# Performance work log

Measured on AMD Instinct MI355X. Metric: run time of the kernel, lower is better.

## Reference

```python
import jax, jax.numpy as jnp
import numpy as np

TOKENS = 32768
D_MODEL = 4096
N_EXPERTS = 64
BALANCE_LOSS_WEIGHT = 0.1


def setup_inputs() -> dict:
    key = jax.random.key(0)
    kx, kw1, kw2, kn = jax.random.split(key, 4)
    x = jax.random.normal(kx, (TOKENS, D_MODEL), dtype=jnp.float32)
    # torch nn.Linear weight layout: [out_features, in_features]
    w1 = jax.random.normal(kw1, (N_EXPERTS, D_MODEL), dtype=jnp.float32) / np.sqrt(D_MODEL)
    w2 = jax.random.normal(kw2, (N_EXPERTS, N_EXPERTS), dtype=jnp.float32) / np.sqrt(N_EXPERTS)
    # fixed Gumbel noise sample: g = -log(-log(u)), matching gumbel_rsample
    u = jax.random.uniform(kn, (TOKENS, N_EXPERTS), dtype=jnp.float32, minval=1e-8, maxval=1.0)
    noise = -jnp.log(-jnp.log(u))
    return {"x": x, "w1": w1, "w2": w2, "noise": noise}


def reference(x, w1, w2, noise):
    # MLP gate: Linear(d->E, no bias) -> tanh -> Linear(E->E, no bias)
    h = jnp.tanh(x @ w1.T)                       # [T, E]
    logits = h @ w2.T                             # [T, E]
    scores = jax.nn.softmax(logits, axis=1)       # [T, E]
    logits_w_noise = logits + noise               # gumbel-perturbed logits
    top1_indices = jnp.argmax(logits_w_noise, axis=1)   # [T] int
    top1_scores = jnp.max(logits_w_noise, axis=1)       # [T]
    # balance loss
    importance_mean = scores.mean(axis=0)                        # [E]
    load = jnp.bincount(top1_indices, length=N_EXPERTS)          # [E] int
    load_mean = load.astype(scores.dtype) / x.shape[0]           # [E]
    balance_loss = (N_EXPERTS * jnp.sum(importance_mean * load_mean)
                    * BALANCE_LOSS_WEIGHT)
    return (top1_indices, top1_scores, balance_loss, load_mean, importance_mean)
```

## Files before the change

### kernel.cpp

```cpp
#include <hip/hip_runtime.h>
#include <math.h>

#define TOKENS 32768
#define DM 4096
#define NE 64
#define BALW 0.1f

#define TG 64
#define GBLOCKS (TOKENS / TG)

typedef __attribute__((ext_vector_type(8))) short short8;
typedef __attribute__((ext_vector_type(4))) float f32x4;

typedef unsigned short us;

__device__ inline us bf16r(float f) {
  const unsigned u = __float_as_uint(f);
  return (us)((u + 0x7FFFu + ((u >> 16) & 1u)) >> 16);
}
__device__ inline float bf16f(us s) {
  return __uint_as_float(((unsigned)s) << 16);
}
__device__ inline void split8(const float4 v0, const float4 v1, short8& H,
                              short8& M, short8& L) {
  float v[8] = {v0.x, v0.y, v0.z, v0.w, v1.x, v1.y, v1.z, v1.w};
#pragma unroll
  for (int j = 0; j < 8; ++j) {
    const us hs = bf16r(v[j]);
    const float r1 = v[j] - bf16f(hs);
    const us ms = bf16r(r1);
    const float r2 = r1 - bf16f(ms);
    const us ls = bf16r(r2);
    H[j] = (short)hs; M[j] = (short)ms; L[j] = (short)ls;
  }
}

__device__ inline void split8t(const float4 v0, const float4 v1, short8& H,
                               short8& M, short8& L) {
  unsigned u[8], um[8], ul[8];
  const float v[8] = {v0.x, v0.y, v0.z, v0.w, v1.x, v1.y, v1.z, v1.w};
#pragma unroll
  for (int j = 0; j < 8; ++j) {
    u[j] = __float_as_uint(v[j]);
    const float r1 = v[j] - __uint_as_float(u[j] & 0xFFFF0000u);
    um[j] = __float_as_uint(r1);
    const float r2 = r1 - __uint_as_float(um[j] & 0xFFFF0000u);
    ul[j] = __float_as_uint(r2);
  }
  union Cvt { unsigned u4[4]; short8 s8; } h, m, l;
#pragma unroll
  for (int d = 0; d < 4; ++d) {
    h.u4[d] = __builtin_amdgcn_perm(u[2 * d + 1], u[2 * d], 0x07060302u);
    m.u4[d] = __builtin_amdgcn_perm(um[2 * d + 1], um[2 * d], 0x07060302u);
    l.u4[d] = __builtin_amdgcn_perm(ul[2 * d + 1], ul[2 * d], 0x07060302u);
  }
  H = h.s8; M = m.s8; L = l.s8;
}

#define MFMA(a, b, c) __builtin_amdgcn_mfma_f32_16x16x32_bf16(a, b, c, 0, 0, 0)

__global__ void prep_w1_kernel(const float* __restrict__ w1,
                               us* __restrict__ bws) {
  const int kc = blockIdx.x;
  const int tid = threadIdx.x;
  const int ns = tid >> 6;
  const int l = tid & 63;
  const int r = l & 15, g = l >> 4;
  const int n = 16 * ns + r;
  const int kb = 32 * kc + 8 * g;
  const float* src = &w1[(size_t)n * DM + kb];
  const float4 v0 = *reinterpret_cast<const float4*>(src);
  const float4 v1 = *reinterpret_cast<const float4*>(src + 4);
  short8 H, M, L;
  split8(v0, v1, H, M, L);
  us* dst = bws + ((size_t)(kc * 4 + ns) * 3) * 512 + l * 8;
  *reinterpret_cast<short8*>(dst) = H;
  *reinterpret_cast<short8*>(dst + 512) = M;
  *reinterpret_cast<short8*>(dst + 1024) = L;
}

#define TMM 128

template <int SK>
__global__ __launch_bounds__(256, 2) void gemm_mfma_kernel(
    const float* __restrict__ x, const us* __restrict__ bws,
    float* __restrict__ hp) {
  constexpr int KS = DM / SK;
  constexpr int NIT = KS / 32;
  const int tid = threadIdx.x;
  const int kz = blockIdx.x % SK;
  const int mb = blockIdx.x / SK;
  const int w = tid >> 6;
  const int l = tid & 63;
  const int r = l & 15, g = l >> 4;
  const int row0 = mb * TMM + w * 32;
  const int kb0 = kz * KS;

  f32x4 acc[2][4];
#pragma unroll
  for (int i = 0; i < 2; ++i)
#pragma unroll
    for (int j = 0; j < 4; ++j) acc[i][j] = (f32x4)(0.f);

  const float* xA0 = &x[(size_t)(row0 + r) * DM + kb0 + 8 * g];
  const float* xA1 = xA0 + (size_t)16 * DM;
  const us* bb = bws + (size_t)(kb0 / 32) * 12 * 512 + l * 8;

  float4 a00 = *reinterpret_cast<const float4*>(xA0);
  float4 a01 = *reinterpret_cast<const float4*>(xA0 + 4);
  float4 a10 = *reinterpret_cast<const float4*>(xA1);
  float4 a11 = *reinterpret_cast<const float4*>(xA1 + 4);
  short8 bf[4][3];
#pragma unroll
  for (int ns = 0; ns < 4; ++ns)
#pragma unroll
    for (int p = 0; p < 3; ++p)
      bf[ns][p] = *reinterpret_cast<const short8*>(bb + (ns * 3 + p) * 512);

  for (int it = 0; it < NIT; ++it) {
    const int itn = (it + 1 < NIT) ? it + 1 : it;
    const us* btn = bb + (size_t)itn * 12 * 512;
    const int ko = itn * 32;
    const float4 n00 = *reinterpret_cast<const float4*>(xA0 + ko);
    const float4 n01 = *reinterpret_cast<const float4*>(xA0 + ko + 4);
    const float4 n10 = *reinterpret_cast<const float4*>(xA1 + ko);
    const float4 n11 = *reinterpret_cast<const float4*>(xA1 + ko + 4);

    short8 ah0, am0, al0, ah1, am1, al1;
    split8t(a00, a01, ah0, am0, al0);
    split8t(a10, a11, ah1, am1, al1);

#define PROW(AH0, AH1, P)                                                \
  do {                                                                   \
    _Pragma("unroll") for (int ns = 0; ns < 4; ++ns) {                   \
      acc[0][ns] = MFMA(AH0, bf[ns][P], acc[0][ns]);                     \
      acc[1][ns] = MFMA(AH1, bf[ns][P], acc[1][ns]);                     \
    }                                                                    \
  } while (0)
#define RELOAD(P)                                                        \
  do {                                                                   \
    _Pragma("unroll") for (int ns = 0; ns < 4; ++ns) bf[ns][P] =         \
        *reinterpret_cast<const short8*>(btn + (ns * 3 + (P)) * 512);    \
  } while (0)

    PROW(ah0, ah1, 0);
    PROW(am0, am1, 0);
    PROW(al0, al1, 0);
    RELOAD(0);
    PROW(ah0, ah1, 1);
    PROW(am0, am1, 1);
    RELOAD(1);
    PROW(ah0, ah1, 2);
    RELOAD(2);
#undef PROW
#undef RELOAD

    a00 = n00; a01 = n01; a10 = n10; a11 = n11;
  }

  float* dst = hp + (size_t)kz * TOKENS * NE;
#pragma unroll
  for (int ms = 0; ms < 2; ++ms)
#pragma unroll
    for (int ns = 0; ns < 4; ++ns)
#pragma unroll
      for (int q = 0; q < 4; ++q)
        dst[(size_t)(row0 + 16 * ms + 4 * g + q) * NE + 16 * ns + r] =
            acc[ms][ns][q];
}

#define TM 128
#define BK 32
#define LDSA 132
#define LDSB 68

template <int SK>
__global__ __launch_bounds__(256, 4) void gemm_fp32_kernel(
    const float* __restrict__ x, const float* __restrict__ w1,
    float* __restrict__ hp) {
  constexpr int KS = DM / SK;
  __shared__ float As[BK * LDSA];
  __shared__ float Ws[BK * LDSB];
  const int tid = threadIdx.x;
  const int kz = blockIdx.x % SK;
  const int mb = blockIdx.x / SK;
  const int row0 = mb * TM;
  const int kbase = kz * KS;
  const int m0 = (tid >> 3) * 4;
  const int n0 = (tid & 7) * 8;
  const int rS = tid >> 2;
  const int kS = (tid & 3) * 4;

  float acc[4][8];
#pragma unroll
  for (int i = 0; i < 4; ++i)
#pragma unroll
    for (int j = 0; j < 8; ++j) acc[i][j] = 0.f;

  float4 ra[4], rw[2];
  const float* xp = &x[(size_t)(row0 + rS) * DM + kS];
  const float* wp = &w1[(size_t)rS * DM + kS];

#define LOAD_TILE(KC)                                                   \
  do {                                                                  \
    ra[0] = *reinterpret_cast<const float4*>(xp + (KC));                \
    ra[1] = *reinterpret_cast<const float4*>(xp + (KC) + 16);           \
    ra[2] = *reinterpret_cast<const float4*>(xp + (size_t)64 * DM + (KC));\
    ra[3] = *reinterpret_cast<const float4*>(xp + (size_t)64 * DM + (KC) + 16);\
    rw[0] = *reinterpret_cast<const float4*>(wp + (KC));                \
    rw[1] = *reinterpret_cast<const float4*>(wp + (KC) + 16);           \
  } while (0)

#define ST4(arr, stride, krow, col, v)                                  \
  do {                                                                  \
    arr[((krow) + 0) * (stride) + (col)] = (v).x;                       \
    arr[((krow) + 1) * (stride) + (col)] = (v).y;                       \
    arr[((krow) + 2) * (stride) + (col)] = (v).z;                       \
    arr[((krow) + 3) * (stride) + (col)] = (v).w;                       \
  } while (0)

#define STORE_TILE()                                                    \
  do {                                                                  \
    ST4(As, LDSA, kS, rS, ra[0]);                                       \
    ST4(As, LDSA, kS + 16, rS, ra[1]);                                  \
    ST4(As, LDSA, kS, rS + 64, ra[2]);                                  \
    ST4(As, LDSA, kS + 16, rS + 64, ra[3]);                             \
    ST4(Ws, LDSB, kS, rS, rw[0]);                                       \
    ST4(Ws, LDSB, kS + 16, rS, rw[1]);                                  \
  } while (0)

  LOAD_TILE(kbase);

  for (int kc = kbase; kc < kbase + KS; kc += BK) {
    __syncthreads();
    STORE_TILE();
    __syncthreads();
    if (kc + BK < kbase + KS) LOAD_TILE(kc + BK);
#pragma unroll 8
    for (int k = 0; k < BK; ++k) {
      const float4 a0 = *reinterpret_cast<const float4*>(&As[k * LDSA + m0]);
      const float4 b0 = *reinterpret_cast<const float4*>(&Ws[k * LDSB + n0]);
      const float4 b1 =
          *reinterpret_cast<const float4*>(&Ws[k * LDSB + n0 + 4]);
      const float a[4] = {a0.x, a0.y, a0.z, a0.w};
      const float b[8] = {b0.x, b0.y, b0.z, b0.w, b1.x, b1.y, b1.z, b1.w};
#pragma unroll
      for (int i = 0; i < 4; ++i)
#pragma unroll
        for (int j = 0; j < 8; ++j) acc[i][j] = fmaf(a[i], b[j], acc[i][j]);
    }
  }
#undef LOAD_TILE
#undef ST4
#undef STORE_TILE

  float* dst = hp + (size_t)kz * TOKENS * NE;
#pragma unroll
  for (int i = 0; i < 4; ++i) {
    const size_t o = (size_t)(row0 + m0 + i) * NE;
    *reinterpret_cast<float4*>(&dst[o + n0]) =
        make_float4(acc[i][0], acc[i][1], acc[i][2], acc[i][3]);
    *reinterpret_cast<float4*>(&dst[o + n0 + 4]) =
        make_float4(acc[i][4], acc[i][5], acc[i][6], acc[i][7]);
  }
}

template <int SK>
__global__ __launch_bounds__(256) void gate_kernel(
    const float* __restrict__ hp, const float* __restrict__ w2,
    const float* __restrict__ noise, float* __restrict__ out_idx,
    float* __restrict__ out_score, float* __restrict__ imp_part,
    float* __restrict__ load_part) {
  __shared__ float hs[TG * 65];
  __shared__ float w2s[NE * 65];
  __shared__ float ls[TG * 66];
  __shared__ float csum[2 * NE];
  __shared__ int hist[NE];
  const int tid = threadIdx.x;
  const int t0 = blockIdx.x * TG;
  if (tid < NE) hist[tid] = 0;

#pragma unroll
  for (int it = 0; it < 4; ++it) {
    const int f = tid + 256 * it;
    const int c = f & 15;
    const int t = f >> 4;
    const size_t g = (size_t)(t0 + t) * NE + c * 4;
    float4 p = *reinterpret_cast<const float4*>(&hp[g]);
#pragma unroll
    for (int s = 1; s < SK; ++s) {
      const float4 q =
          *reinterpret_cast<const float4*>(&hp[(size_t)s * TOKENS * NE + g]);
      p.x += q.x; p.y += q.y; p.z += q.z; p.w += q.w;
    }
    float* d = &hs[t * 65 + c * 4];
    d[0] = tanhf(p.x);
    d[1] = tanhf(p.y);
    d[2] = tanhf(p.z);
    d[3] = tanhf(p.w);
  }
#pragma unroll
  for (int it = 0; it < 4; ++it) {
    const int f = tid + 256 * it;
    const int c = f & 15;
    const int rr = f >> 4;
    const float4 v =
        *reinterpret_cast<const float4*>(&w2[(size_t)rr * NE + c * 4]);
    float* d = &w2s[rr * 65 + c * 4];
    d[0] = v.x; d[1] = v.y; d[2] = v.z; d[3] = v.w;
  }
  __syncthreads();

  {
    const int m0 = (tid >> 4) * 4;
    const int n0 = (tid & 15) * 4;
    float acc[4][4];
#pragma unroll
    for (int i = 0; i < 4; ++i)
#pragma unroll
      for (int j = 0; j < 4; ++j) acc[i][j] = 0.f;
#pragma unroll 8
    for (int k = 0; k < NE; ++k) {
      float a[4], b[4];
#pragma unroll
      for (int i = 0; i < 4; ++i) a[i] = hs[(m0 + i) * 65 + k];
#pragma unroll
      for (int j = 0; j < 4; ++j) b[j] = w2s[(n0 + j) * 65 + k];
#pragma unroll
      for (int i = 0; i < 4; ++i)
#pragma unroll
        for (int j = 0; j < 4; ++j) acc[i][j] = fmaf(a[i], b[j], acc[i][j]);
    }
#pragma unroll
    for (int i = 0; i < 4; ++i)
#pragma unroll
      for (int j = 0; j < 4; ++j) ls[(m0 + i) * 66 + n0 + j] = acc[i][j];
  }
  __syncthreads();

  if (tid < TG) {
    const int t = tid;
    float mx = -INFINITY, best = -INFINITY;
    int bi = 0;
    for (int e = 0; e < NE; ++e) {
      const float lv = ls[t * 66 + e];
      mx = fmaxf(mx, lv);
      const float gg = lv + noise[(size_t)(t0 + t) * NE + e];
      if (gg > best) { best = gg; bi = e; }
    }
    float s = 0.f;
    for (int e = 0; e < NE; ++e) {
      const float ex = expf(ls[t * 66 + e] - mx);
      s += ex;
      ls[t * 66 + e] = ex;
    }
    const float inv = 1.f / s;
    for (int e = 0; e < NE; ++e) ls[t * 66 + e] *= inv;
    out_idx[t0 + t] = (float)bi;
    out_score[t0 + t] = best;
    atomicAdd(&hist[bi], 1);
  }
  __syncthreads();

  if (tid < 128) {
    const int e = tid & 63;
    const int half = tid >> 6;
    float s = 0.f;
    for (int rr = half * 32; rr < half * 32 + 32; ++rr) s += ls[rr * 66 + e];
    csum[half * NE + e] = s;
  }
  __syncthreads();
  if (tid < NE) {
    imp_part[(size_t)blockIdx.x * NE + tid] = csum[tid] + csum[NE + tid];
    load_part[(size_t)blockIdx.x * NE + tid] = (float)hist[tid];
  }
}

__global__ void finalize_kernel(const float* __restrict__ imp_part,
                                const float* __restrict__ load_part,
                                float* __restrict__ out) {
  const int e = threadIdx.x;
  float imp = 0.f, ld = 0.f;
  for (int b = 0; b < GBLOCKS; ++b) {
    imp += imp_part[(size_t)b * NE + e];
    ld += load_part[(size_t)b * NE + e];
  }
  const float imp_mean = imp / (float)TOKENS;
  const float load_mean = ld / (float)TOKENS;
  out[2 * TOKENS + 1 + e] = load_mean;
  out[2 * TOKENS + 1 + NE + e] = imp_mean;
  float prod = imp_mean * load_mean;
#pragma unroll
  for (int off = 32; off > 0; off >>= 1) prod += __shfl_down(prod, off);
  if (e == 0) out[2 * TOKENS] = (float)NE * prod * BALW;
}

extern "C" void kernel_launch(void* const* d_in, const int* in_sizes, int n_in,
                              void* d_out, int out_size, void* d_ws,
                              size_t ws_size, hipStream_t stream) {
  const float* x = (const float*)d_in[0];
  const float* w1 = (const float*)d_in[1];
  const float* w2 = (const float*)d_in[2];
  const float* noise = (const float*)d_in[3];
  float* out = (float*)d_out;

  const size_t bws_shorts = (size_t)128 * 4 * 3 * 512;
  const size_t part_elems = (size_t)2 * GBLOCKS * NE;
  const size_t need_mfma = bws_shorts * sizeof(us) +
                           ((size_t)2 * TOKENS * NE + part_elems) *
                               sizeof(float);
  const size_t need_fp32 =
      ((size_t)2 * TOKENS * NE + part_elems) * sizeof(float);

  if (ws_size == 0 || ws_size >= need_mfma) {
    us* bws = (us*)d_ws;
    float* hp = (float*)(bws + bws_shorts);
    float* imp_part = hp + (size_t)2 * TOKENS * NE;
    float* load_part = imp_part + (size_t)GBLOCKS * NE;
    hipLaunchKernelGGL(prep_w1_kernel, dim3(128), dim3(256), 0, stream, w1,
                       bws);
    hipLaunchKernelGGL((gemm_mfma_kernel<2>), dim3((TOKENS / TMM) * 2),
                       dim3(256), 0, stream, x, bws, hp);
    hipLaunchKernelGGL((gate_kernel<2>), dim3(GBLOCKS), dim3(256), 0, stream,
                       hp, w2, noise, out, out + TOKENS, imp_part, load_part);
    hipLaunchKernelGGL(finalize_kernel, dim3(1), dim3(64), 0, stream, imp_part,
                       load_part, out);
  } else if (ws_size >= need_fp32) {
    float* hp = (float*)d_ws;
    float* imp_part = hp + (size_t)2 * TOKENS * NE;
    float* load_part = imp_part + (size_t)GBLOCKS * NE;
    hipLaunchKernelGGL((gemm_fp32_kernel<2>), dim3((TOKENS / TM) * 2),
                       dim3(256), 0, stream, x, w1, hp);
    hipLaunchKernelGGL((gate_kernel<2>), dim3(GBLOCKS), dim3(256), 0, stream,
                       hp, w2, noise, out, out + TOKENS, imp_part, load_part);
    hipLaunchKernelGGL(finalize_kernel, dim3(1), dim3(64), 0, stream, imp_part,
                       load_part, out);
  }
}
```

Measured before the change: 202.3 us.

## Double MFMA row tile per wave, parallelize gate softmax and finalize reduction

Each wave in the MFMA GEMM now covers 64 rows instead of 32, so every B-fragment register load feeds twice as many MFMAs. This halves the grid and raises register pressure. The gate kernel's softmax/argmax pass now uses all 256 threads, four per token, with the partial results combined through shared memory. The finalize kernel now reduces the per-block partials with 1024 threads instead of 64.

```diff
diff --git a/kernel.cpp b/kernel.cpp
--- a/kernel.cpp
+++ b/kernel.cpp
@@ -79,7 +79,7 @@
   *reinterpret_cast<short8*>(dst + 1024) = L;
 }
 
-#define TMM 128
+#define TMM 256
 
 template <int SK>
 __global__ __launch_bounds__(256, 2) void gemm_mfma_kernel(
@@ -93,23 +93,27 @@
   const int w = tid >> 6;
   const int l = tid & 63;
   const int r = l & 15, g = l >> 4;
-  const int row0 = mb * TMM + w * 32;
+  const int wrow0 = mb * TMM + w * 64;
   const int kb0 = kz * KS;
 
-  f32x4 acc[2][4];
-#pragma unroll
-  for (int i = 0; i < 2; ++i)
+  f32x4 acc[4][4];
+#pragma unroll
+  for (int i = 0; i < 4; ++i)
 #pragma unroll
     for (int j = 0; j < 4; ++j) acc[i][j] = (f32x4)(0.f);
 
-  const float* xA0 = &x[(size_t)(row0 + r) * DM + kb0 + 8 * g];
-  const float* xA1 = xA0 + (size_t)16 * DM;
+  const float* xA[4];
+#pragma unroll
+  for (int rg = 0; rg < 4; ++rg)
+    xA[rg] = &x[(size_t)(wrow0 + 16 * rg + r) * DM + kb0 + 8 * g];
   const us* bb = bws + (size_t)(kb0 / 32) * 12 * 512 + l * 8;
 
-  float4 a00 = *reinterpret_cast<const float4*>(xA0);
-  float4 a01 = *reinterpret_cast<const float4*>(xA0 + 4);
-  float4 a10 = *reinterpret_cast<const float4*>(xA1);
-  float4 a11 = *reinterpret_cast<const float4*>(xA1 + 4);
+  float4 ac[4][2], an[4][2];
+#pragma unroll
+  for (int rg = 0; rg < 4; ++rg) {
+    ac[rg][0] = *reinterpret_cast<const float4*>(xA[rg]);
+    ac[rg][1] = *reinterpret_cast<const float4*>(xA[rg] + 4);
+  }
   short8 bf[4][3];
 #pragma unroll
   for (int ns = 0; ns < 4; ++ns)
@@ -121,20 +125,17 @@
     const int itn = (it + 1 < NIT) ? it + 1 : it;
     const us* btn = bb + (size_t)itn * 12 * 512;
     const int ko = itn * 32;
-    const float4 n00 = *reinterpret_cast<const float4*>(xA0 + ko);
-    const float4 n01 = *reinterpret_cast<const float4*>(xA0 + ko + 4);
-    const float4 n10 = *reinterpret_cast<const float4*>(xA1 + ko);
-    const float4 n11 = *reinterpret_cast<const float4*>(xA1 + ko + 4);
-
-    short8 ah0, am0, al0, ah1, am1, al1;
-    split8t(a00, a01, ah0, am0, al0);
-    split8t(a10, a11, ah1, am1, al1);
-
-#define PROW(AH0, AH1, P)                                                \
+#pragma unroll
+    for (int rg = 0; rg < 4; ++rg) {
+      an[rg][0] = *reinterpret_cast<const float4*>(xA[rg] + ko);
+      an[rg][1] = *reinterpret_cast<const float4*>(xA[rg] + ko + 4);
+    }
+
+#define PROW2(AH0, AH1, R0, R1, P)                                       \
   do {                                                                   \
     _Pragma("unroll") for (int ns = 0; ns < 4; ++ns) {                   \
-      acc[0][ns] = MFMA(AH0, bf[ns][P], acc[0][ns]);                     \
-      acc[1][ns] = MFMA(AH1, bf[ns][P], acc[1][ns]);                     \
+      acc[R0][ns] = MFMA(AH0, bf[ns][P], acc[R0][ns]);                   \
+      acc[R1][ns] = MFMA(AH1, bf[ns][P], acc[R1][ns]);                   \
     }                                                                    \
   } while (0)
 #define RELOAD(P)                                                        \
@@ -143,30 +144,45 @@
         *reinterpret_cast<const short8*>(btn + (ns * 3 + (P)) * 512);    \
   } while (0)
 
-    PROW(ah0, ah1, 0);
-    PROW(am0, am1, 0);
-    PROW(al0, al1, 0);
+    short8 ah0, am0, al0, ah1, am1, al1;
+    split8t(ac[0][0], ac[0][1], ah0, am0, al0);
+    split8t(ac[1][0], ac[1][1], ah1, am1, al1);
+    PROW2(ah0, ah1, 0, 1, 0);
+    PROW2(am0, am1, 0, 1, 0);
+    PROW2(al0, al1, 0, 1, 0);
+    PROW2(ah0, ah1, 0, 1, 1);
+    PROW2(am0, am1, 0, 1, 1);
+    PROW2(ah0, ah1, 0, 1, 2);
+    split8t(ac[2][0], ac[2][1], ah0, am0, al0);
+    split8t(ac[3][0], ac[3][1], ah1, am1, al1);
+    PROW2(ah0, ah1, 2, 3, 0);
+    PROW2(am0, am1, 2, 3, 0);
+    PROW2(al0, al1, 2, 3, 0);
     RELOAD(0);
-    PROW(ah0, ah1, 1);
-    PROW(am0, am1, 1);
+    PROW2(ah0, ah1, 2, 3, 1);
+    PROW2(am0, am1, 2, 3, 1);
     RELOAD(1);
-    PROW(ah0, ah1, 2);
+    PROW2(ah0, ah1, 2, 3, 2);
     RELOAD(2);
-#undef PROW
+#undef PROW2
 #undef RELOAD
 
-    a00 = n00; a01 = n01; a10 = n10; a11 = n11;
+#pragma unroll
+    for (int rg = 0; rg < 4; ++rg) {
+      ac[rg][0] = an[rg][0];
+      ac[rg][1] = an[rg][1];
+    }
   }
 
   float* dst = hp + (size_t)kz * TOKENS * NE;
 #pragma unroll
-  for (int ms = 0; ms < 2; ++ms)
+  for (int rg = 0; rg < 4; ++rg)
 #pragma unroll
     for (int ns = 0; ns < 4; ++ns)
 #pragma unroll
       for (int q = 0; q < 4; ++q)
-        dst[(size_t)(row0 + 16 * ms + 4 * g + q) * NE + 16 * ns + r] =
-            acc[ms][ns][q];
+        dst[(size_t)(wrow0 + 16 * rg + 4 * g + q) * NE + 16 * ns + r] =
+            acc[rg][ns][q];
 }
 
 #define TM 128
@@ -276,6 +292,10 @@
   __shared__ float ls[TG * 66];
   __shared__ float csum[2 * NE];
   __shared__ int hist[NE];
+  __shared__ float cmax[4][TG];
+  __shared__ float cbest[4][TG];
+  __shared__ int cbi[4][TG];
+  __shared__ float csub[4][TG];
   const int tid = threadIdx.x;
   const int t0 = blockIdx.x * TG;
   if (tid < NE) hist[tid] = 0;
@@ -338,27 +358,44 @@
   }
   __syncthreads();
 
-  if (tid < TG) {
-    const int t = tid;
+  {
+    const int t = tid & 63;
+    const int q = tid >> 6;
     float mx = -INFINITY, best = -INFINITY;
-    int bi = 0;
-    for (int e = 0; e < NE; ++e) {
+    int bi = 16 * q;
+    for (int i = 0; i < 16; ++i) {
+      const int e = 16 * q + i;
       const float lv = ls[t * 66 + e];
       mx = fmaxf(mx, lv);
       const float gg = lv + noise[(size_t)(t0 + t) * NE + e];
       if (gg > best) { best = gg; bi = e; }
     }
+    cmax[q][t] = mx; cbest[q][t] = best; cbi[q][t] = bi;
+    __syncthreads();
+    const float fmx = fmaxf(fmaxf(cmax[0][t], cmax[1][t]),
+                            fmaxf(cmax[2][t], cmax[3][t]));
     float s = 0.f;
-    for (int e = 0; e < NE; ++e) {
-      const float ex = expf(ls[t * 66 + e] - mx);
+    for (int i = 0; i < 16; ++i) {
+      const int e = 16 * q + i;
+      const float ex = expf(ls[t * 66 + e] - fmx);
       s += ex;
       ls[t * 66 + e] = ex;
     }
-    const float inv = 1.f / s;
-    for (int e = 0; e < NE; ++e) ls[t * 66 + e] *= inv;
-    out_idx[t0 + t] = (float)bi;
-    out_score[t0 + t] = best;
-    atomicAdd(&hist[bi], 1);
+    csub[q][t] = s;
+    __syncthreads();
+    const float inv =
+        1.f / (csub[0][t] + csub[1][t] + csub[2][t] + csub[3][t]);
+    for (int i = 0; i < 16; ++i) ls[t * 66 + 16 * q + i] *= inv;
+    if (tid < TG) {
+      float fb = -INFINITY;
+      int fbi = 0;
+#pragma unroll
+      for (int qq = 0; qq < 4; ++qq)
+        if (cbest[qq][t] > fb) { fb = cbest[qq][t]; fbi = cbi[qq][t]; }
+      out_idx[t0 + t] = (float)fbi;
+      out_score[t0 + t] = fb;
+      atomicAdd(&hist[fbi], 1);
+    }
   }
   __syncthreads();
 
@@ -379,20 +416,32 @@
 __global__ void finalize_kernel(const float* __restrict__ imp_part,
                                 const float* __restrict__ load_part,
                                 float* __restrict__ out) {
-  const int e = threadIdx.x;
+  __shared__ float si[16][NE];
+  __shared__ float sl[16][NE];
+  const int tid = threadIdx.x;
+  const int e = tid & 63;
+  const int seg = tid >> 6;
   float imp = 0.f, ld = 0.f;
-  for (int b = 0; b < GBLOCKS; ++b) {
+  for (int b = seg; b < GBLOCKS; b += 16) {
     imp += imp_part[(size_t)b * NE + e];
     ld += load_part[(size_t)b * NE + e];
   }
-  const float imp_mean = imp / (float)TOKENS;
-  const float load_mean = ld / (float)TOKENS;
-  out[2 * TOKENS + 1 + e] = load_mean;
-  out[2 * TOKENS + 1 + NE + e] = imp_mean;
-  float prod = imp_mean * load_mean;
-#pragma unroll
-  for (int off = 32; off > 0; off >>= 1) prod += __shfl_down(prod, off);
-  if (e == 0) out[2 * TOKENS] = (float)NE * prod * BALW;
+  si[seg][e] = imp;
+  sl[seg][e] = ld;
+  __syncthreads();
+  if (tid < NE) {
+    float ti = 0.f, tl = 0.f;
+#pragma unroll
+    for (int s = 0; s < 16; ++s) { ti += si[s][tid]; tl += sl[s][tid]; }
+    const float imp_mean = ti / (float)TOKENS;
+    const float load_mean = tl / (float)TOKENS;
+    out[2 * TOKENS + 1 + tid] = load_mean;
+    out[2 * TOKENS + 1 + NE + tid] = imp_mean;
+    float prod = imp_mean * load_mean;
+#pragma unroll
+    for (int off = 32; off > 0; off >>= 1) prod += __shfl_down(prod, off);
+    if (tid == 0) out[2 * TOKENS] = (float)NE * prod * BALW;
+  }
 }
 
 extern "C" void kernel_launch(void* const* d_in, const int* in_sizes, int n_in,
@@ -423,8 +472,8 @@
                        dim3(256), 0, stream, x, bws, hp);
     hipLaunchKernelGGL((gate_kernel<2>), dim3(GBLOCKS), dim3(256), 0, stream,
                        hp, w2, noise, out, out + TOKENS, imp_part, load_part);
-    hipLaunchKernelGGL(finalize_kernel, dim3(1), dim3(64), 0, stream, imp_part,
-                       load_part, out);
+    hipLaunchKernelGGL(finalize_kernel, dim3(1), dim3(1024), 0, stream,
+                       imp_part, load_part, out);
   } else if (ws_size >= need_fp32) {
     float* hp = (float*)d_ws;
     float* imp_part = hp + (size_t)2 * TOKENS * NE;
@@ -433,7 +482,7 @@
                        dim3(256), 0, stream, x, w1, hp);
     hipLaunchKernelGGL((gate_kernel<2>), dim3(GBLOCKS), dim3(256), 0, stream,
                        hp, w2, noise, out, out + TOKENS, imp_part, load_part);
-    hipLaunchKernelGGL(finalize_kernel, dim3(1), dim3(64), 0, stream, imp_part,
-                       load_part, out);
-  }
-}
+    hipLaunchKernelGGL(finalize_kernel, dim3(1), dim3(1024), 0, stream,
+                       imp_part, load_part, out);
+  }
+}
```

New measurement: 226.7 us. 1.12x slower.
